# Performance work log

Hardware: AMD Instinct MI355X
Metric: run time of the kernel (lower is better)

## Reference

```python
import jax, jax.numpy as jnp
import numpy as np

N_NODES = 100000


def _add_self_loops(edge_index, num_nodes):
    loops = jnp.arange(num_nodes, dtype=edge_index.dtype)
    src = jnp.concatenate([edge_index[0], loops])
    dst = jnp.concatenate([edge_index[1], loops])
    return src, dst


def _gcn_norm(src, dst, num_nodes, dtype):
    # symmetric normalization D^-1/2 (A+I) D^-1/2 with unit edge weights
    ones = jnp.ones(dst.shape[0], dtype=dtype)
    deg = jax.ops.segment_sum(ones, dst, num_segments=num_nodes)
    dinv = jnp.where(deg > 0, jax.lax.rsqrt(deg), 0.0).astype(dtype)
    return dinv[src] * dinv[dst]  # [E+N]


def _gcn_conv(x, W, b, src, dst, norm, num_nodes):
    h = x @ W                                  # [N, C] dense transform
    msg = h[src] * norm[:, None]               # [E+N, C] gather + scale
    agg = jax.ops.segment_sum(msg, dst, num_segments=num_nodes)  # scatter-add
    return agg + b


def setup_inputs() -> dict:
    key = jax.random.key(0)
    k1, k2, k3, k4 = jax.random.split(key, 4)
    F = 128
    C = 128
    E = 1600000
    x = jax.random.normal(k1, (N_NODES, F), dtype=jnp.float32)
    edge_index = jax.random.randint(k2, (2, E), 0, N_NODES, dtype=jnp.int64)
    s = 1.0 / np.sqrt(F)
    W1 = jax.random.normal(k3, (F, C), dtype=jnp.float32) * s
    b1 = jnp.zeros((C,), dtype=jnp.float32)
    W2 = jax.random.normal(k4, (C, C), dtype=jnp.float32) * s
    b2 = jnp.zeros((C,), dtype=jnp.float32)
    return {"x": x, "edge_index": edge_index, "W1": W1, "b1": b1, "W2": W2, "b2": b2}


def reference(x, edge_index, W1, b1, W2, b2):
    num_nodes = x.shape[0]
    src, dst = _add_self_loops(edge_index, num_nodes)
    norm = _gcn_norm(src, dst, num_nodes, x.dtype)  # cached=True: same for both layers
    h = _gcn_conv(x, W1, b1, src, dst, norm, num_nodes)
    h = _gcn_conv(h, W2, b2, src, dst, norm, num_nodes)
    return jax.nn.relu(h)  # relu only at the end, per original forward
```

## Files before the change

### kernel.cpp

```cpp
#include <hip/hip_runtime.h>


#define WS_ALIGN(x) (((x) + 255) & ~(size_t)255)
#define BINSH 9
#define EPB 4096

typedef __attribute__((ext_vector_type(8))) short bf16x8;
typedef __attribute__((ext_vector_type(4))) float f32x4;
typedef _Float16 f16x8 __attribute__((ext_vector_type(8)));
typedef _Float16 f16x4 __attribute__((ext_vector_type(4)));

__device__ inline ushort bf16rn(float f) {
    uint u = __float_as_uint(f);
    u = (u + 0x7FFFu + ((u >> 16) & 1u)) >> 16;
    return (ushort)u;
}
__device__ inline float bf16tof(ushort h) {
    return __uint_as_float(((uint)h) << 16);
}

__global__ void k_hist(const int* __restrict__ src, const int* __restrict__ dst,
                       int* __restrict__ hist, int E, int N, int nbins, int nblocksB) {
    __shared__ int h[256];
    int tid = threadIdx.x;
    h[tid] = 0;
    __syncthreads();
    int e0 = blockIdx.x * EPB;
#pragma unroll
    for (int i = 0; i < EPB / 256; ++i) {
        int e = e0 + i * 256 + tid;
        if (e < E) {
            int d = dst[e];
            int s = src[e];
            if ((unsigned)d < (unsigned)N && (unsigned)s < (unsigned)N)
                atomicAdd(&h[d >> BINSH], 1);
        }
    }
    __syncthreads();
    if (tid < nbins) hist[tid * nblocksB + blockIdx.x] = h[tid];
}

__global__ void k_scanA(const int* __restrict__ in, int* __restrict__ outv,
                        int* __restrict__ bsums, int L) {
    __shared__ int sh[256];
    int i = blockIdx.x * 256 + threadIdx.x;
    int v = (i < L) ? in[i] : 0;
    sh[threadIdx.x] = v;
    __syncthreads();
    for (int off = 1; off < 256; off <<= 1) {
        int t = (threadIdx.x >= off) ? sh[threadIdx.x - off] : 0;
        __syncthreads();
        sh[threadIdx.x] += t;
        __syncthreads();
    }
    if (i < L) outv[i] = sh[threadIdx.x] - v;
    if (threadIdx.x == 255) bsums[blockIdx.x] = sh[255];
}

__global__ void k_scan2(int* __restrict__ bsums, int nb) {
    __shared__ int sh[512];
    int tid = threadIdx.x;
    int v = (tid < nb) ? bsums[tid] : 0;
    sh[tid] = v;
    __syncthreads();
    for (int off = 1; off < 512; off <<= 1) {
        int t = (tid >= off) ? sh[tid - off] : 0;
        __syncthreads();
        sh[tid] += t;
        __syncthreads();
    }
    if (tid < nb) bsums[tid] = sh[tid] - v;
}

__global__ void k_scanB(int* __restrict__ outv, const int* __restrict__ bsums, int L) {
    int i = blockIdx.x * 256 + threadIdx.x;
    if (i < L) outv[i] += bsums[blockIdx.x];
}

__global__ void k_part(const int* __restrict__ src, const int* __restrict__ dst,
                       const int* __restrict__ hists, uint* __restrict__ part,
                       int E, int N, int nbins, int nblocksB) {
    __shared__ int cur[256];
    int tid = threadIdx.x;
    if (tid < nbins) cur[tid] = hists[tid * nblocksB + blockIdx.x];
    __syncthreads();
    int e0 = blockIdx.x * EPB;
#pragma unroll
    for (int i = 0; i < EPB / 256; ++i) {
        int e = e0 + i * 256 + tid;
        if (e < E) {
            int d = dst[e];
            int s = src[e];
            if ((unsigned)d < (unsigned)N && (unsigned)s < (unsigned)N) {
                int pos = atomicAdd(&cur[d >> BINSH], 1);
                part[pos] = (uint)s | ((uint)(d & 511) << 23);
            }
        }
    }
}

__global__ void k_bin(const uint* __restrict__ part, const int* __restrict__ hists,
                      const int* __restrict__ hist, int nbins, int nblocksB, int N,
                      int* __restrict__ csr, int* __restrict__ offs,
                      float* __restrict__ dinv) {
    __shared__ int cnt[512];
    __shared__ int loff[512];
    __shared__ int ps[256];
    int b = blockIdx.x;
    int tid = threadIdx.x;
    int start = hists[b * nblocksB];
    int last = nbins * nblocksB - 1;
    int end = (b + 1 < nbins) ? hists[(b + 1) * nblocksB] : (hists[last] + hist[last]);

    cnt[tid] = 0;
    cnt[tid + 256] = 0;
    __syncthreads();
    for (int i = start + tid; i < end; i += 256)
        atomicAdd(&cnt[part[i] >> 23], 1);
    __syncthreads();

    int a0 = cnt[2 * tid], a1 = cnt[2 * tid + 1];
    ps[tid] = a0 + a1;
    __syncthreads();
    for (int off = 1; off < 256; off <<= 1) {
        int t = (tid >= off) ? ps[tid - off] : 0;
        __syncthreads();
        ps[tid] += t;
        __syncthreads();
    }
    int excl = ps[tid] - (a0 + a1);
    loff[2 * tid] = excl;
    loff[2 * tid + 1] = excl + a0;
    __syncthreads();

    int d0 = b << BINSH;
#pragma unroll
    for (int h = 0; h < 2; ++h) {
        int k = tid + h * 256;
        int d = d0 + k;
        if (d < N) {
            offs[d] = start + loff[k];
            dinv[d] = rsqrtf((float)(cnt[k] + 1));
        }
    }
    if (b == nbins - 1 && tid == 0) offs[N] = end;
    __syncthreads();

    for (int i = start + tid; i < end; i += 256) {
        uint p = part[i];
        int pos = atomicAdd(&loff[p >> 23], 1);
        csr[start + pos] = (int)(p & 0x7FFFFFu);
    }
}

__global__ void k_conv_w12(const float* __restrict__ x, const float* __restrict__ dinv,
                           ushort* __restrict__ xh, int N,
                           const float* __restrict__ W1, const float* __restrict__ b1,
                           const float* __restrict__ W2,
                           float* __restrict__ w12, float* __restrict__ cvec, int cb) {
    int bid = blockIdx.x;
    if (bid < cb) {
        int tid = bid * 256 + threadIdx.x;
        int stride = cb * 256;
        int n4 = N * 32;
        for (int i = tid; i < n4; i += stride) {
            float4 v = ((const float4*)x)[i];
            float di = dinv[i >> 5];
            f16x4 h;
            h[0] = (_Float16)(di * v.x);
            h[1] = (_Float16)(di * v.y);
            h[2] = (_Float16)(di * v.z);
            h[3] = (_Float16)(di * v.w);
            ((uint2*)xh)[i] = __builtin_bit_cast(uint2, h);
        }
    } else if (bid < cb + 64) {
        int idx = (bid - cb) * 256 + threadIdx.x;
        int i = idx >> 7, j = idx & 127;
        float s = 0.f;
#pragma unroll 8
        for (int k = 0; k < 128; ++k) s = fmaf(W1[i * 128 + k], W2[k * 128 + j], s);
        w12[idx] = s;
    } else {
        int j = threadIdx.x;
        if (j < 128) {
            float s = 0.f;
#pragma unroll 8
            for (int k = 0; k < 128; ++k) s = fmaf(b1[k], W2[k * 128 + j], s);
            cvec[j] = s;
        }
    }
}

template <int WRITE_Q>
__launch_bounds__(256)
__global__ void k_aggq(const ushort* __restrict__ xh, const float* __restrict__ dinv,
                       float* __restrict__ fout, ushort* __restrict__ qout,
                       float* __restrict__ svec,
                       const int* __restrict__ offs, const int* __restrict__ csr, int N) {
    int wid = (int)((blockIdx.x * (size_t)blockDim.x + threadIdx.x) >> 6);
    int lane = threadIdx.x & 63;
    int gwA = 2 * wid, gwB = 2 * wid + 1;
    if (gwA >= N) return;
    bool vB = (gwB < N);
    int q = lane >> 4, ql = lane & 15;
    float diA = dinv[gwA];
    float diB = vB ? dinv[gwB] : 0.f;
    const uint4* __restrict__ xh4 = (const uint4*)xh;

    float accA[8], accB[8];
#pragma unroll
    for (int j = 0; j < 8; ++j) { accA[j] = 0.f; accB[j] = 0.f; }
    float sdA = 0.f, sdB = 0.f;

    if (q == 0) {
        uint4 va = xh4[((size_t)gwA << 4) + ql];
        f16x8 ha = __builtin_bit_cast(f16x8, va);
#pragma unroll
        for (int j = 0; j < 8; ++j) accA[j] = (float)ha[j];
        if (vB) {
            uint4 vb = xh4[((size_t)gwB << 4) + ql];
            f16x8 hb = __builtin_bit_cast(f16x8, vb);
#pragma unroll
            for (int j = 0; j < 8; ++j) accB[j] = (float)hb[j];
        }
    }

    int s0A = offs[gwA], s1A = offs[gwA + 1];
    int s0B = s1A;
    int s1B = vB ? offs[gwB + 1] : s1A;

    int baseA = s0A, baseB = s0B;
    while (baseA < s1A || baseB < s1B) {
        int cA = s1A - baseA; cA = cA < 0 ? 0 : (cA > 64 ? 64 : cA);
        int cB = s1B - baseB; cB = cB < 0 ? 0 : (cB > 64 ? 64 : cB);
        int sidxA = 0, sidxB = 0;
        if (lane < cA) sidxA = csr[baseA + lane];
        if (lane < cB) sidxB = csr[baseB + lane];
        if (WRITE_Q) {
            if (lane < cA) sdA += dinv[sidxA];
            if (lane < cB) sdB += dinv[sidxB];
        }
        int itA = (cA + 3) >> 2, itB = (cB + 3) >> 2;
        int iters = itA > itB ? itA : itB;
#pragma unroll 2
        for (int i = 0; i < iters; ++i) {
            int t = 4 * i + q;
            int sA = __shfl(sidxA, t);
            int sB = __shfl(sidxB, t);
            if (t < cA) {
                uint4 v = xh4[((size_t)sA << 4) + ql];
                f16x8 h = __builtin_bit_cast(f16x8, v);
#pragma unroll
                for (int j = 0; j < 8; ++j) accA[j] += (float)h[j];
            }
            if (t < cB) {
                uint4 v = xh4[((size_t)sB << 4) + ql];
                f16x8 h = __builtin_bit_cast(f16x8, v);
#pragma unroll
                for (int j = 0; j < 8; ++j) accB[j] += (float)h[j];
            }
        }
        baseA += 64;
        baseB += 64;
    }

#pragma unroll
    for (int j = 0; j < 8; ++j) {
        accA[j] += __shfl_xor(accA[j], 16);
        accA[j] += __shfl_xor(accA[j], 32);
        accB[j] += __shfl_xor(accB[j], 16);
        accB[j] += __shfl_xor(accB[j], 32);
    }

    if (WRITE_Q) {
#pragma unroll
        for (int d = 1; d < 64; d <<= 1) {
            sdA += __shfl_xor(sdA, d);
            sdB += __shfl_xor(sdB, d);
        }
        if (lane == 0) {
            svec[gwA] = diA * (diA + sdA);
            if (vB) svec[gwB] = diB * (diB + sdB);
        }
        if (q == 0) {
            float fA = diA * diA, fB = diB * diB;
            f16x8 ha, hb;
#pragma unroll
            for (int j = 0; j < 8; ++j) {
                ha[j] = (_Float16)(fA * accA[j]);
                hb[j] = (_Float16)(fB * accB[j]);
            }
            *(uint4*)(qout + (size_t)gwA * 128 + ql * 8) = __builtin_bit_cast(uint4, ha);
            if (vB) *(uint4*)(qout + (size_t)gwB * 128 + ql * 8) = __builtin_bit_cast(uint4, hb);
        }
    } else {
        if (q == 0) {
            float4 o0, o1, p0, p1;
            o0.x = diA * accA[0]; o0.y = diA * accA[1]; o0.z = diA * accA[2]; o0.w = diA * accA[3];
            o1.x = diA * accA[4]; o1.y = diA * accA[5]; o1.z = diA * accA[6]; o1.w = diA * accA[7];
            *(float4*)(fout + (size_t)gwA * 128 + ql * 8) = o0;
            *(float4*)(fout + (size_t)gwA * 128 + ql * 8 + 4) = o1;
            if (vB) {
                p0.x = diB * accB[0]; p0.y = diB * accB[1]; p0.z = diB * accB[2]; p0.w = diB * accB[3];
                p1.x = diB * accB[4]; p1.y = diB * accB[5]; p1.z = diB * accB[6]; p1.w = diB * accB[7];
                *(float4*)(fout + (size_t)gwB * 128 + ql * 8) = p0;
                *(float4*)(fout + (size_t)gwB * 128 + ql * 8 + 4) = p1;
            }
        }
    }
}

__global__ void k_wpack(const float* __restrict__ w12,
                        ushort* __restrict__ wph, ushort* __restrict__ wpl) {
    int idx = blockIdx.x * 256 + threadIdx.x;
    int lane = idx & 63;
    int kb = (idx >> 6) & 3;
    int nt = idx >> 8;
    int n = nt * 16 + (lane & 15);
    int k0 = kb * 32 + (lane >> 4) * 8;
    ushort h[8], l[8];
#pragma unroll
    for (int i = 0; i < 8; ++i) {
        float f = w12[(k0 + i) * 128 + n];
        h[i] = bf16rn(f);
        l[i] = bf16rn(f - bf16tof(h[i]));
    }
    uint4 oh, ol;
    oh.x = (uint)h[0] | ((uint)h[1] << 16);
    oh.y = (uint)h[2] | ((uint)h[3] << 16);
    oh.z = (uint)h[4] | ((uint)h[5] << 16);
    oh.w = (uint)h[6] | ((uint)h[7] << 16);
    ol.x = (uint)l[0] | ((uint)l[1] << 16);
    ol.y = (uint)l[2] | ((uint)l[3] << 16);
    ol.z = (uint)l[4] | ((uint)l[5] << 16);
    ol.w = (uint)l[6] | ((uint)l[7] << 16);
    ((uint4*)wph)[idx] = oh;
    ((uint4*)wpl)[idx] = ol;
}

__launch_bounds__(256)
__global__ void k_gemm_mfma(const float* __restrict__ X,
                            const ushort* __restrict__ wph, const ushort* __restrict__ wpl,
                            const float* __restrict__ svec, const float* __restrict__ cvec,
                            const float* __restrict__ b2, float* __restrict__ out, int N) {
    __shared__ uint4 wsh[2048];
    __shared__ uint4 wsl[2048];
    int tid = threadIdx.x;
    int lane = tid & 63;
    int wv = tid >> 6;
    int row0 = blockIdx.x * 128;

#pragma unroll
    for (int it = 0; it < 8; ++it) {
        wsh[it * 256 + tid] = ((const uint4*)wph)[it * 256 + tid];
        wsl[it * 256 + tid] = ((const uint4*)wpl)[it * 256 + tid];
    }

    bf16x8 ah[2][4], al[2][4];
#pragma unroll
    for (int s = 0; s < 2; ++s) {
#pragma unroll
        for (int kb = 0; kb < 4; ++kb) {
            int row = row0 + wv * 32 + s * 16 + (lane & 15);
            int kbase = kb * 32 + (lane >> 4) * 8;
            float f[8];
            if (row < N) {
                float4 a = *(const float4*)(X + (size_t)row * 128 + kbase);
                float4 b = *(const float4*)(X + (size_t)row * 128 + kbase + 4);
                f[0] = a.x; f[1] = a.y; f[2] = a.z; f[3] = a.w;
                f[4] = b.x; f[5] = b.y; f[6] = b.z; f[7] = b.w;
            } else {
#pragma unroll
                for (int i = 0; i < 8; ++i) f[i] = 0.f;
            }
            bf16x8 hh, ll;
#pragma unroll
            for (int i = 0; i < 8; ++i) {
                ushort h = bf16rn(f[i]);
                hh[i] = (short)h;
                ll[i] = (short)bf16rn(f[i] - bf16tof(h));
            }
            ah[s][kb] = hh;
            al[s][kb] = ll;
        }
    }
    __syncthreads();

    f32x4 acc[2][8];
#pragma unroll
    for (int s = 0; s < 2; ++s)
#pragma unroll
        for (int nt = 0; nt < 8; ++nt) acc[s][nt] = (f32x4)(0.f);

#pragma unroll
    for (int nt = 0; nt < 8; ++nt) {
#pragma unroll
        for (int kb = 0; kb < 4; ++kb) {
            uint4 rh = wsh[(nt * 4 + kb) * 64 + lane];
            uint4 rl = wsl[(nt * 4 + kb) * 64 + lane];
            bf16x8 bh = __builtin_bit_cast(bf16x8, rh);
            bf16x8 bl = __builtin_bit_cast(bf16x8, rl);
            acc[0][nt] = __builtin_amdgcn_mfma_f32_16x16x32_bf16(ah[0][kb], bh, acc[0][nt], 0, 0, 0);
            acc[0][nt] = __builtin_amdgcn_mfma_f32_16x16x32_bf16(al[0][kb], bh, acc[0][nt], 0, 0, 0);
            acc[0][nt] = __builtin_amdgcn_mfma_f32_16x16x32_bf16(ah[0][kb], bl, acc[0][nt], 0, 0, 0);
            acc[1][nt] = __builtin_amdgcn_mfma_f32_16x16x32_bf16(ah[1][kb], bh, acc[1][nt], 0, 0, 0);
            acc[1][nt] = __builtin_amdgcn_mfma_f32_16x16x32_bf16(al[1][kb], bh, acc[1][nt], 0, 0, 0);
            acc[1][nt] = __builtin_amdgcn_mfma_f32_16x16x32_bf16(ah[1][kb], bl, acc[1][nt], 0, 0, 0);
        }
    }

    float cv[8], bv[8];
#pragma unroll
    for (int nt = 0; nt < 8; ++nt) {
        cv[nt] = cvec[nt * 16 + (lane & 15)];
        bv[nt] = b2[nt * 16 + (lane & 15)];
    }
#pragma unroll
    for (int s = 0; s < 2; ++s) {
#pragma unroll
        for (int r = 0; r < 4; ++r) {
            int row = row0 + wv * 32 + s * 16 + (lane >> 4) * 4 + r;
            if (row < N) {
                float sv = svec[row];
#pragma unroll
                for (int nt = 0; nt < 8; ++nt) {
                    float o = fmaxf(acc[s][nt][r] + sv * cv[nt] + bv[nt], 0.f);
                    out[(size_t)row * 128 + nt * 16 + (lane & 15)] = o;
                }
            }
        }
    }
}

extern "C" void kernel_launch(void* const* d_in, const int* in_sizes, int n_in,
                              void* d_out, int out_size, void* d_ws, size_t ws_size,
                              hipStream_t stream) {
    const float* x  = (const float*)d_in[0];
    const int*   ei = (const int*)d_in[1];
    const float* W1 = (const float*)d_in[2];
    const float* b1 = (const float*)d_in[3];
    const float* W2 = (const float*)d_in[4];
    const float* b2 = (const float*)d_in[5];
    float* out = (float*)d_out;

    int N = in_sizes[0] / 128;
    int E = in_sizes[1] / 2;
    const int* srcE = ei;
    const int* dstE = ei + E;

    int nbins = (N + 511) >> BINSH;
    int nblocksB = (E + EPB - 1) / EPB;
    int L = nbins * nblocksB;
    int nbL = (L + 255) / 256;

    char* w = (char*)d_ws;
    size_t off = 0;
    auto alloc = [&](size_t bytes) {
        void* p = w + off;
        off = WS_ALIGN(off + bytes);
        return p;
    };
    ushort* xh    = (ushort*)alloc((size_t)N * 256);
    ushort* t1h   = (ushort*)alloc((size_t)N * 256);
    int*   csr    = (int*)alloc((size_t)E * 4);
    int*   hist   = (int*)alloc((size_t)L * 4);
    int*   hists  = (int*)alloc((size_t)L * 4);
    int*   bsums  = (int*)alloc(4096);
    int*   offs   = (int*)alloc((size_t)(N + 1) * 4);
    float* dinv   = (float*)alloc((size_t)N * 4);
    float* svec   = (float*)alloc((size_t)N * 4);
    float* w12    = (float*)alloc(128 * 128 * 4);
    ushort* wph   = (ushort*)alloc(128 * 128 * 2);
    ushort* wpl   = (ushort*)alloc(128 * 128 * 2);
    float* cvec   = (float*)alloc(128 * 4);
    (void)ws_size; (void)n_in; (void)out_size;

    uint* part = (uint*)t1h;

    k_hist<<<nblocksB, 256, 0, stream>>>(srcE, dstE, hist, E, N, nbins, nblocksB);
    k_scanA<<<nbL, 256, 0, stream>>>(hist, hists, bsums, L);
    k_scan2<<<1, 512, 0, stream>>>(bsums, nbL);
    k_scanB<<<nbL, 256, 0, stream>>>(hists, bsums, L);
    k_part<<<nblocksB, 256, 0, stream>>>(srcE, dstE, hists, part, E, N, nbins, nblocksB);
    k_bin<<<nbins, 256, 0, stream>>>(part, hists, hist, nbins, nblocksB, N,
                                     csr, offs, dinv);
    k_conv_w12<<<512 + 65, 256, 0, stream>>>(x, dinv, xh, N, W1, b1, W2, w12, cvec, 512);
    k_aggq<1><<<(N + 7) / 8, 256, 0, stream>>>(xh, dinv, nullptr, t1h, svec,
                                               offs, csr, N);
    k_aggq<0><<<(N + 7) / 8, 256, 0, stream>>>(t1h, dinv, out, nullptr, nullptr,
                                               offs, csr, N);
    k_wpack<<<8, 256, 0, stream>>>(w12, wph, wpl);
    k_gemm_mfma<<<(N + 127) / 128, 256, 0, stream>>>(out, wph, wpl, svec, cvec, b2, out, N);
}
```

Baseline: 229.8 us.

## Fuse preprocessing kernels and move dinv scaling into first aggregation

The x-to-fp16 conversion and the W1·W2 / b1·W2 products are folded into the histogram kernel, since they no longer depend on dinv. The first aggregation now applies dinv per source node inside its gather loop. The scanB pass is dropped by adding block sums at read time in the partition and bin kernels, and the weight packing is merged into the partition kernel. This removes three launches and lets independent work overlap. In exchange, the first aggregation does an extra shuffle and FMA per edge, and x is now stored unscaled in fp16.

```diff
diff --git a/kernel.cpp b/kernel.cpp
--- a/kernel.cpp
+++ b/kernel.cpp
@@ -19,25 +19,60 @@
     return __uint_as_float(((uint)h) << 16);
 }
 
-__global__ void k_hist(const int* __restrict__ src, const int* __restrict__ dst,
-                       int* __restrict__ hist, int E, int N, int nbins, int nblocksB) {
-    __shared__ int h[256];
+__global__ void k_hist_fused(const int* __restrict__ src, const int* __restrict__ dst,
+                             int* __restrict__ hist, int E, int N, int nbins, int hb,
+                             const float* __restrict__ x, ushort* __restrict__ xh,
+                             const float* __restrict__ W1, const float* __restrict__ b1,
+                             const float* __restrict__ W2,
+                             float* __restrict__ w12, float* __restrict__ cvec, int cb) {
+    int bid = blockIdx.x;
     int tid = threadIdx.x;
-    h[tid] = 0;
-    __syncthreads();
-    int e0 = blockIdx.x * EPB;
-#pragma unroll
-    for (int i = 0; i < EPB / 256; ++i) {
-        int e = e0 + i * 256 + tid;
-        if (e < E) {
-            int d = dst[e];
-            int s = src[e];
-            if ((unsigned)d < (unsigned)N && (unsigned)s < (unsigned)N)
-                atomicAdd(&h[d >> BINSH], 1);
-        }
-    }
-    __syncthreads();
-    if (tid < nbins) hist[tid * nblocksB + blockIdx.x] = h[tid];
+    if (bid < hb) {
+        __shared__ int h[256];
+        h[tid] = 0;
+        __syncthreads();
+        int e0 = bid * EPB;
+#pragma unroll
+        for (int i = 0; i < EPB / 256; ++i) {
+            int e = e0 + i * 256 + tid;
+            if (e < E) {
+                int d = dst[e];
+                int s = src[e];
+                if ((unsigned)d < (unsigned)N && (unsigned)s < (unsigned)N)
+                    atomicAdd(&h[d >> BINSH], 1);
+            }
+        }
+        __syncthreads();
+        if (tid < nbins) hist[tid * hb + bid] = h[tid];
+    } else if (bid < hb + cb) {
+        int t = (bid - hb) * 256 + tid;
+        int stride = cb * 256;
+        int n4 = N * 32;
+        for (int i = t; i < n4; i += stride) {
+            float4 v = ((const float4*)x)[i];
+            f16x4 hh;
+            hh[0] = (_Float16)v.x;
+            hh[1] = (_Float16)v.y;
+            hh[2] = (_Float16)v.z;
+            hh[3] = (_Float16)v.w;
+            ((uint2*)xh)[i] = __builtin_bit_cast(uint2, hh);
+        }
+    } else if (bid < hb + cb + 64) {
+        int idx = (bid - hb - cb) * 256 + tid;
+        int i = idx >> 7, j = idx & 127;
+        float s = 0.f;
+#pragma unroll 8
+        for (int k = 0; k < 128; ++k) s = fmaf(W1[i * 128 + k], W2[k * 128 + j], s);
+        w12[idx] = s;
+    } else {
+        int j = tid;
+        if (j < 128) {
+            float s = 0.f;
+#pragma unroll 8
+            for (int k = 0; k < 128; ++k) s = fmaf(b1[k], W2[k * 128 + j], s);
+            cvec[j] = s;
+        }
+    }
 }
 
 __global__ void k_scanA(const int* __restrict__ in, int* __restrict__ outv,
@@ -72,35 +107,64 @@
     if (tid < nb) bsums[tid] = sh[tid] - v;
 }
 
-__global__ void k_scanB(int* __restrict__ outv, const int* __restrict__ bsums, int L) {
-    int i = blockIdx.x * 256 + threadIdx.x;
-    if (i < L) outv[i] += bsums[blockIdx.x];
-}
-
-__global__ void k_part(const int* __restrict__ src, const int* __restrict__ dst,
-                       const int* __restrict__ hists, uint* __restrict__ part,
-                       int E, int N, int nbins, int nblocksB) {
-    __shared__ int cur[256];
+__global__ void k_part_fused(const int* __restrict__ src, const int* __restrict__ dst,
+                             const int* __restrict__ hists, const int* __restrict__ bsums,
+                             uint* __restrict__ part, int E, int N, int nbins, int pb,
+                             const float* __restrict__ w12,
+                             ushort* __restrict__ wph, ushort* __restrict__ wpl) {
+    int bid = blockIdx.x;
     int tid = threadIdx.x;
-    if (tid < nbins) cur[tid] = hists[tid * nblocksB + blockIdx.x];
-    __syncthreads();
-    int e0 = blockIdx.x * EPB;
-#pragma unroll
-    for (int i = 0; i < EPB / 256; ++i) {
-        int e = e0 + i * 256 + tid;
-        if (e < E) {
-            int d = dst[e];
-            int s = src[e];
-            if ((unsigned)d < (unsigned)N && (unsigned)s < (unsigned)N) {
-                int pos = atomicAdd(&cur[d >> BINSH], 1);
-                part[pos] = (uint)s | ((uint)(d & 511) << 23);
-            }
-        }
+    if (bid < pb) {
+        __shared__ int cur[256];
+        if (tid < nbins) {
+            int fi = tid * pb + bid;
+            cur[tid] = hists[fi] + bsums[fi >> 8];
+        }
+        __syncthreads();
+        int e0 = bid * EPB;
+#pragma unroll
+        for (int i = 0; i < EPB / 256; ++i) {
+            int e = e0 + i * 256 + tid;
+            if (e < E) {
+                int d = dst[e];
+                int s = src[e];
+                if ((unsigned)d < (unsigned)N && (unsigned)s < (unsigned)N) {
+                    int pos = atomicAdd(&cur[d >> BINSH], 1);
+                    part[pos] = (uint)s | ((uint)(d & 511) << 23);
+                }
+            }
+        }
+    } else {
+        int idx = (bid - pb) * 256 + tid;
+        int lane = idx & 63;
+        int kb = (idx >> 6) & 3;
+        int nt = idx >> 8;
+        int n = nt * 16 + (lane & 15);
+        int k0 = kb * 32 + (lane >> 4) * 8;
+        ushort h[8], l[8];
+#pragma unroll
+        for (int i = 0; i < 8; ++i) {
+            float f = w12[(k0 + i) * 128 + n];
+            h[i] = bf16rn(f);
+            l[i] = bf16rn(f - bf16tof(h[i]));
+        }
+        uint4 oh, ol;
+        oh.x = (uint)h[0] | ((uint)h[1] << 16);
+        oh.y = (uint)h[2] | ((uint)h[3] << 16);
+        oh.z = (uint)h[4] | ((uint)h[5] << 16);
+        oh.w = (uint)h[6] | ((uint)h[7] << 16);
+        ol.x = (uint)l[0] | ((uint)l[1] << 16);
+        ol.y = (uint)l[2] | ((uint)l[3] << 16);
+        ol.z = (uint)l[4] | ((uint)l[5] << 16);
+        ol.w = (uint)l[6] | ((uint)l[7] << 16);
+        ((uint4*)wph)[idx] = oh;
+        ((uint4*)wpl)[idx] = ol;
     }
 }
 
 __global__ void k_bin(const uint* __restrict__ part, const int* __restrict__ hists,
-                      const int* __restrict__ hist, int nbins, int nblocksB, int N,
+                      const int* __restrict__ bsums, const int* __restrict__ hist,
+                      int nbins, int nblocksB, int N,
                       int* __restrict__ csr, int* __restrict__ offs,
                       float* __restrict__ dinv) {
     __shared__ int cnt[512];
@@ -108,9 +172,16 @@
     __shared__ int ps[256];
     int b = blockIdx.x;
     int tid = threadIdx.x;
-    int start = hists[b * nblocksB];
+    int fi0 = b * nblocksB;
+    int start = hists[fi0] + bsums[fi0 >> 8];
     int last = nbins * nblocksB - 1;
-    int end = (b + 1 < nbins) ? hists[(b + 1) * nblocksB] : (hists[last] + hist[last]);
+    int end;
+    if (b + 1 < nbins) {
+        int fi1 = (b + 1) * nblocksB;
+        end = hists[fi1] + bsums[fi1 >> 8];
+    } else {
+        end = hists[last] + bsums[last >> 8] + hist[last];
+    }
 
     cnt[tid] = 0;
     cnt[tid + 256] = 0;
@@ -150,44 +221,6 @@
         uint p = part[i];
         int pos = atomicAdd(&loff[p >> 23], 1);
         csr[start + pos] = (int)(p & 0x7FFFFFu);
-    }
-}
-
-__global__ void k_conv_w12(const float* __restrict__ x, const float* __restrict__ dinv,
-                           ushort* __restrict__ xh, int N,
-                           const float* __restrict__ W1, const float* __restrict__ b1,
-                           const float* __restrict__ W2,
-                           float* __restrict__ w12, float* __restrict__ cvec, int cb) {
-    int bid = blockIdx.x;
-    if (bid < cb) {
-        int tid = bid * 256 + threadIdx.x;
-        int stride = cb * 256;
-        int n4 = N * 32;
-        for (int i = tid; i < n4; i += stride) {
-            float4 v = ((const float4*)x)[i];
-            float di = dinv[i >> 5];
-            f16x4 h;
-            h[0] = (_Float16)(di * v.x);
-            h[1] = (_Float16)(di * v.y);
-            h[2] = (_Float16)(di * v.z);
-            h[3] = (_Float16)(di * v.w);
-            ((uint2*)xh)[i] = __builtin_bit_cast(uint2, h);
-        }
-    } else if (bid < cb + 64) {
-        int idx = (bid - cb) * 256 + threadIdx.x;
-        int i = idx >> 7, j = idx & 127;
-        float s = 0.f;
-#pragma unroll 8
-        for (int k = 0; k < 128; ++k) s = fmaf(W1[i * 128 + k], W2[k * 128 + j], s);
-        w12[idx] = s;
-    } else {
-        int j = threadIdx.x;
-        if (j < 128) {
-            float s = 0.f;
-#pragma unroll 8
-            for (int k = 0; k < 128; ++k) s = fmaf(b1[k], W2[k * 128 + j], s);
-            cvec[j] = s;
-        }
     }
 }
 
@@ -215,13 +248,15 @@
     if (q == 0) {
         uint4 va = xh4[((size_t)gwA << 4) + ql];
         f16x8 ha = __builtin_bit_cast(f16x8, va);
-#pragma unroll
-        for (int j = 0; j < 8; ++j) accA[j] = (float)ha[j];
+        float wA = WRITE_Q ? diA : 1.f;
+#pragma unroll
+        for (int j = 0; j < 8; ++j) accA[j] = wA * (float)ha[j];
         if (vB) {
             uint4 vb = xh4[((size_t)gwB << 4) + ql];
             f16x8 hb = __builtin_bit_cast(f16x8, vb);
-#pragma unroll
-            for (int j = 0; j < 8; ++j) accB[j] = (float)hb[j];
+            float wB = WRITE_Q ? diB : 1.f;
+#pragma unroll
+            for (int j = 0; j < 8; ++j) accB[j] = wB * (float)hb[j];
         }
     }
 
@@ -234,11 +269,12 @@
         int cA = s1A - baseA; cA = cA < 0 ? 0 : (cA > 64 ? 64 : cA);
         int cB = s1B - baseB; cB = cB < 0 ? 0 : (cB > 64 ? 64 : cB);
         int sidxA = 0, sidxB = 0;
+        float dvA = 0.f, dvB = 0.f;
         if (lane < cA) sidxA = csr[baseA + lane];
         if (lane < cB) sidxB = csr[baseB + lane];
         if (WRITE_Q) {
-            if (lane < cA) sdA += dinv[sidxA];
-            if (lane < cB) sdB += dinv[sidxB];
+            if (lane < cA) { dvA = dinv[sidxA]; sdA += dvA; }
+            if (lane < cB) { dvB = dinv[sidxB]; sdB += dvB; }
         }
         int itA = (cA + 3) >> 2, itB = (cB + 3) >> 2;
         int iters = itA > itB ? itA : itB;
@@ -247,17 +283,25 @@
             int t = 4 * i + q;
             int sA = __shfl(sidxA, t);
             int sB = __shfl(sidxB, t);
+            float dA = 0.f, dB = 0.f;
+            if (WRITE_Q) { dA = __shfl(dvA, t); dB = __shfl(dvB, t); }
             if (t < cA) {
                 uint4 v = xh4[((size_t)sA << 4) + ql];
                 f16x8 h = __builtin_bit_cast(f16x8, v);
 #pragma unroll
-                for (int j = 0; j < 8; ++j) accA[j] += (float)h[j];
+                for (int j = 0; j < 8; ++j) {
+                    if (WRITE_Q) accA[j] = fmaf(dA, (float)h[j], accA[j]);
+                    else         accA[j] += (float)h[j];
+                }
             }
             if (t < cB) {
                 uint4 v = xh4[((size_t)sB << 4) + ql];
                 f16x8 h = __builtin_bit_cast(f16x8, v);
 #pragma unroll
-                for (int j = 0; j < 8; ++j) accB[j] += (float)h[j];
+                for (int j = 0; j < 8; ++j) {
+                    if (WRITE_Q) accB[j] = fmaf(dB, (float)h[j], accB[j]);
+                    else         accB[j] += (float)h[j];
+                }
             }
         }
         baseA += 64;
@@ -308,34 +352,6 @@
             }
         }
     }
-}
-
-__global__ void k_wpack(const float* __restrict__ w12,
-                        ushort* __restrict__ wph, ushort* __restrict__ wpl) {
-    int idx = blockIdx.x * 256 + threadIdx.x;
-    int lane = idx & 63;
-    int kb = (idx >> 6) & 3;
-    int nt = idx >> 8;
-    int n = nt * 16 + (lane & 15);
-    int k0 = kb * 32 + (lane >> 4) * 8;
-    ushort h[8], l[8];
-#pragma unroll
-    for (int i = 0; i < 8; ++i) {
-        float f = w12[(k0 + i) * 128 + n];
-        h[i] = bf16rn(f);
-        l[i] = bf16rn(f - bf16tof(h[i]));
-    }
-    uint4 oh, ol;
-    oh.x = (uint)h[0] | ((uint)h[1] << 16);
-    oh.y = (uint)h[2] | ((uint)h[3] << 16);
-    oh.z = (uint)h[4] | ((uint)h[5] << 16);
-    oh.w = (uint)h[6] | ((uint)h[7] << 16);
-    ol.x = (uint)l[0] | ((uint)l[1] << 16);
-    ol.y = (uint)l[2] | ((uint)l[3] << 16);
-    ol.z = (uint)l[4] | ((uint)l[5] << 16);
-    ol.w = (uint)l[6] | ((uint)l[7] << 16);
-    ((uint4*)wph)[idx] = oh;
-    ((uint4*)wpl)[idx] = ol;
 }
 
 __launch_bounds__(256)
@@ -477,18 +493,19 @@
 
     uint* part = (uint*)t1h;
 
-    k_hist<<<nblocksB, 256, 0, stream>>>(srcE, dstE, hist, E, N, nbins, nblocksB);
+    int cb = 512;
+    k_hist_fused<<<nblocksB + cb + 65, 256, 0, stream>>>(srcE, dstE, hist, E, N, nbins,
+                                                         nblocksB, x, xh, W1, b1, W2,
+                                                         w12, cvec, cb);
     k_scanA<<<nbL, 256, 0, stream>>>(hist, hists, bsums, L);
     k_scan2<<<1, 512, 0, stream>>>(bsums, nbL);
-    k_scanB<<<nbL, 256, 0, stream>>>(hists, bsums, L);
-    k_part<<<nblocksB, 256, 0, stream>>>(srcE, dstE, hists, part, E, N, nbins, nblocksB);
-    k_bin<<<nbins, 256, 0, stream>>>(part, hists, hist, nbins, nblocksB, N,
+    k_part_fused<<<nblocksB + 8, 256, 0, stream>>>(srcE, dstE, hists, bsums, part,
+                                                   E, N, nbins, nblocksB, w12, wph, wpl);
+    k_bin<<<nbins, 256, 0, stream>>>(part, hists, bsums, hist, nbins, nblocksB, N,
                                      csr, offs, dinv);
-    k_conv_w12<<<512 + 65, 256, 0, stream>>>(x, dinv, xh, N, W1, b1, W2, w12, cvec, 512);
     k_aggq<1><<<(N + 7) / 8, 256, 0, stream>>>(xh, dinv, nullptr, t1h, svec,
                                                offs, csr, N);
     k_aggq<0><<<(N + 7) / 8, 256, 0, stream>>>(t1h, dinv, out, nullptr, nullptr,
                                                offs, csr, N);
-    k_wpack<<<8, 256, 0, stream>>>(w12, wph, wpl);
     k_gemm_mfma<<<(N + 127) / 128, 256, 0, stream>>>(out, wph, wpl, svec, cvec, b2, out, N);
 }
```

New measurement: 222.9 us. 3.0% less time.
